# Performance work log

Measured on AMD Instinct MI355X. Metric: run time of the kernel, lower is better.

Reference implementation:

```python
import jax, jax.numpy as jnp
import numpy as np

INPUT_SIZE = 4096
HIDDEN = 1024
WINDOW = 2048
STRIDE = 1024
METRIC = 32
POOLING = "last"


def setup_inputs() -> dict:
    key = jax.random.key(0)
    ks = jax.random.split(key, 9)
    s = 1.0 / np.sqrt(HIDDEN)  # torch LSTMCell/Linear init bound
    u = lambda k, shape: jax.random.uniform(k, shape, jnp.float32, -s, s)
    return {
        "inp": jax.random.normal(ks[0], (WINDOW, INPUT_SIZE), jnp.float32),
        "h1": jax.random.normal(ks[1], (1, HIDDEN), jnp.float32),
        "c1": jax.random.normal(ks[2], (1, HIDDEN), jnp.float32),
        "W_ih": u(ks[3], (4 * HIDDEN, INPUT_SIZE)),
        "W_hh": u(ks[4], (4 * HIDDEN, HIDDEN)),
        "b_ih": u(ks[5], (4 * HIDDEN,)),
        "b_hh": u(ks[6], (4 * HIDDEN,)),
        "fc_w": u(ks[7], (METRIC, HIDDEN)),
        "fc_b": u(ks[8], (METRIC,)),
    }


def reference(inp, h1, c1, W_ih, W_hh, b_ih, b_hh, fc_w, fc_b):
    window = min(WINDOW, inp.shape[0])
    # Precompute the input-side gate projection as one GEMM: [T, 4H]
    xg = inp[:window] @ W_ih.T + b_ih

    def step(carry, xg_t):
        h, c = carry  # each [1, H]
        gates = xg_t + h @ W_hh.T + b_hh  # [1, 4H]
        i, f, g, o = jnp.split(gates, 4, axis=-1)
        c = jax.nn.sigmoid(f) * c + jax.nn.sigmoid(i) * jnp.tanh(g)
        h = jax.nn.sigmoid(o) * jnp.tanh(c)
        return (h, c), (h, c)

    (h_fin, c_fin), (hs, cs) = jax.lax.scan(step, (h1, c1), xg)

    if window >= STRIDE:
        h_last = jax.lax.stop_gradient(hs[STRIDE - 1])  # [1, H], detached
        c_last = jax.lax.stop_gradient(cs[STRIDE - 1])
    else:
        h_last, c_last = None, None

    if POOLING == "mean":
        # mean of fc(h_i) over last STRIDE steps of the window
        out = (hs[window - STRIDE:, 0, :] @ fc_w.T + fc_b).sum(axis=0, keepdims=True) / STRIDE
    else:  # 'last'
        out = h_fin @ fc_w.T + fc_b  # [1, METRIC]
    out = jnp.tanh(out)
    return out, h_last, c_last
```

## Files before the change

kernel.cpp:

```cpp
#include <hip/hip_runtime.h>
#include <stdint.h>

typedef unsigned short u16;
typedef unsigned long long u64;
typedef __attribute__((ext_vector_type(8))) short short8;
typedef __attribute__((ext_vector_type(4))) float floatx4;

#define K_IN    4096
#define HID     1024
#define G4H     4096
#define T_STEPS 2048
#define NWG     128
#define SPIN_MAX 60000

__device__ __forceinline__ u16 f2bf(float f) {
  union { float f; unsigned int i; } v; v.f = f;
  unsigned int lsb = (v.i >> 16) & 1u;
  v.i += 0x7fffu + lsb;
  return (u16)(v.i >> 16);
}
__device__ __forceinline__ float finz(float x) {
  unsigned b = __float_as_uint(x);
  return ((b & 0x7f800000u) == 0x7f800000u) ? 0.f : x;
}
__device__ __forceinline__ float sigm(float x) {
  x = fminf(30.f, fmaxf(-30.f, finz(x)));
  return 1.0f / (1.0f + __expf(-x));
}
__device__ __forceinline__ float tanh_s(float x) {
  x = fminf(15.f, fmaxf(-15.f, finz(x)));
  float e = __expf(2.0f * x);
  return (e - 1.0f) / (e + 1.0f);
}

__device__ __forceinline__ void publish_h(u64* hx, int slot, int idx, float h) {
  h = finz(h);
  u64 v = ((u64)(unsigned)(slot + 1) << 32) | (u64)__float_as_uint(h);
  __hip_atomic_store(&hx[(size_t)slot * HID + idx], v,
                     __ATOMIC_RELAXED, __HIP_MEMORY_SCOPE_AGENT);
}

#define HXLD(addr) __hip_atomic_load((addr), __ATOMIC_RELAXED, __HIP_MEMORY_SCOPE_AGENT)

__device__ __forceinline__ void poll2(const u64* hx, int slot, int j0,
                                      float* v, int* alive) {
  const u64* p = hx + (size_t)slot * HID + j0;
  const unsigned tag = (unsigned)(slot + 1);
  if (*alive) {
    u64 a0 = HXLD(&p[0]), b0 = HXLD(&p[1]);
    u64 a1 = HXLD(&p[0]), b1 = HXLD(&p[1]);
    int spins = 0;
    for (;;) {
      u64 a2 = HXLD(&p[0]), b2 = HXLD(&p[1]);
      if ((unsigned)(a0 >> 32) == tag && (unsigned)(b0 >> 32) == tag) {
        v[0] = finz(__uint_as_float((unsigned)a0));
        v[1] = finz(__uint_as_float((unsigned)b0));
        return;
      }
      a0 = a1; b0 = b1; a1 = a2; b1 = b2;
      if (++spins > SPIN_MAX) { *alive = 0; break; }
    }
  }
  v[0] = v[1] = 0.f;
}

__global__ __launch_bounds__(256) void cvt_bf16_k(const float* __restrict__ src,
                                                  u16* __restrict__ dst, int n4) {
  int i = blockIdx.x * 256 + threadIdx.x;
  if (i < n4) {
    float4 v = *(const float4*)(src + (size_t)i * 4);
    u16 o0 = f2bf(v.x), o1 = f2bf(v.y), o2 = f2bf(v.z), o3 = f2bf(v.w);
    ushort4 o = {o0, o1, o2, o3};
    *(ushort4*)(dst + (size_t)i * 4) = o;
  }
}

__global__ __launch_bounds__(256) void xg_gemm_k(const u16* __restrict__ A,
                                                 const u16* __restrict__ B,
                                                 const float* __restrict__ bias,
                                                 float* __restrict__ C)
{
  __shared__ __align__(16) u16 As[128 * 64];
  __shared__ __align__(16) u16 Bs[128 * 64];
  const int tid  = threadIdx.x;
  const int lane = tid & 63;
  const int quad = lane >> 4;
  const int l16  = lane & 15;
  const int wid  = tid >> 6;
  const int wm   = wid >> 1, wn = wid & 1;
  const int tileM = blockIdx.y * 128;
  const int tileN = blockIdx.x * 128;

  floatx4 acc[4][4];
  #pragma unroll
  for (int mi = 0; mi < 4; ++mi)
    #pragma unroll
    for (int ni = 0; ni < 4; ++ni)
      acc[mi][ni] = (floatx4){0.f, 0.f, 0.f, 0.f};

  for (int k0 = 0; k0 < K_IN; k0 += 64) {
    #pragma unroll
    for (int i = 0; i < 4; ++i) {
      int c = i * 256 + tid;
      int row = c >> 3, col = (c & 7) * 8;
      *(short8*)(As + c * 8) = *(const short8*)(A + (size_t)(tileM + row) * K_IN + k0 + col);
      *(short8*)(Bs + c * 8) = *(const short8*)(B + (size_t)(tileN + row) * K_IN + k0 + col);
    }
    __syncthreads();
    #pragma unroll
    for (int kk = 0; kk < 64; kk += 32) {
      short8 av[4], bv[4];
      #pragma unroll
      for (int mi = 0; mi < 4; ++mi)
        av[mi] = *(const short8*)(As + (wm * 64 + mi * 16 + l16) * 64 + kk + quad * 8);
      #pragma unroll
      for (int ni = 0; ni < 4; ++ni)
        bv[ni] = *(const short8*)(Bs + (wn * 64 + ni * 16 + l16) * 64 + kk + quad * 8);
      #pragma unroll
      for (int mi = 0; mi < 4; ++mi)
        #pragma unroll
        for (int ni = 0; ni < 4; ++ni)
          acc[mi][ni] = __builtin_amdgcn_mfma_f32_16x16x32_bf16(av[mi], bv[ni], acc[mi][ni], 0, 0, 0);
    }
    __syncthreads();
  }
  #pragma unroll
  for (int ni = 0; ni < 4; ++ni) {
    int n = tileN + wn * 64 + ni * 16 + l16;
    float bn = bias[n];
    #pragma unroll
    for (int mi = 0; mi < 4; ++mi) {
      int mbase = tileM + wm * 64 + mi * 16 + quad * 4;
      #pragma unroll
      for (int r = 0; r < 4; ++r)
        C[(size_t)(mbase + r) * G4H + n] = acc[mi][ni][r] + bn;
    }
  }
}

__global__ __launch_bounds__(512, 1) void lstm_scan_k(const float* __restrict__ Whh,
                                                      const float* __restrict__ bhh,
                                                      const float* __restrict__ h1,
                                                      const float* __restrict__ c1,
                                                      const float* __restrict__ fcw,
                                                      const float* __restrict__ fcb,
                                                      const float* __restrict__ xg,
                                                      u64* hx,
                                                      float* out)
{
  const int g    = blockIdx.x;
  const int tid  = threadIdx.x;
  const int lane = tid & 63;
  const int w    = tid >> 6;
  const int u    = g * 8 + w;

  __shared__ __align__(16) float h_local[HID];
  __shared__ float gsum2[32];
  __shared__ float xgb[2][32];
  __shared__ float bhhb[32];
  __shared__ float pp[32][16];

  floatx4 wreg[4][4];
  #pragma unroll
  for (int q = 0; q < 4; ++q) {
    const float* wr = Whh + (size_t)(q * HID + u) * HID;
    #pragma unroll
    for (int j = 0; j < 4; ++j)
      wreg[q][j] = *(const floatx4*)(wr + j * 256 + lane * 4);
  }
  if (tid < 32) bhhb[tid] = bhh[(tid >> 3) * HID + g * 8 + (tid & 7)];

  float c_state = 0.f;
  if (tid < 8) {
    c_state = c1[g * 8 + tid];
    publish_h(hx, 0, g * 8 + tid, h1[g * 8 + tid]);
  }

  int alive = 1;
  const int j0 = tid * 2;
  for (int t = 0; t < T_STEPS; ++t) {
    float xval = 0.f;
    if (tid < 32) xval = finz(xg[(size_t)t * G4H + (tid >> 3) * HID + g * 8 + (tid & 7)]);
    float v[2];
    poll2(hx, t, j0, v, &alive);
    h_local[j0 + 0] = v[0]; h_local[j0 + 1] = v[1];
    if (tid < 32) xgb[t & 1][tid] = xval;
    __syncthreads();

    float s0 = 0.f, s1 = 0.f, s2 = 0.f, s3 = 0.f;
    #pragma unroll
    for (int j = 0; j < 4; ++j) {
      floatx4 hv = *(const floatx4*)(h_local + j * 256 + lane * 4);
      #pragma unroll
      for (int k = 0; k < 4; ++k) {
        s0 = fmaf(wreg[0][j][k], hv[k], s0);
        s1 = fmaf(wreg[1][j][k], hv[k], s1);
        s2 = fmaf(wreg[2][j][k], hv[k], s2);
        s3 = fmaf(wreg[3][j][k], hv[k], s3);
      }
    }

#define DPP_LEVEL(mods) \
    asm("v_add_f32 %0, %0, %0 " mods : "+v"(s0)); \
    asm("v_add_f32 %0, %0, %0 " mods : "+v"(s1)); \
    asm("v_add_f32 %0, %0, %0 " mods : "+v"(s2)); \
    asm("v_add_f32 %0, %0, %0 " mods : "+v"(s3));
    DPP_LEVEL("row_shr:1 bound_ctrl:0")
    DPP_LEVEL("row_shr:2 bound_ctrl:0")
    DPP_LEVEL("row_shr:4 bank_mask:0xe")
    DPP_LEVEL("row_shr:8 bank_mask:0xc")
    DPP_LEVEL("row_bcast:15 row_mask:0xa")
    DPP_LEVEL("row_bcast:31 row_mask:0xc")
#undef DPP_LEVEL
    if (lane == 63) {
      gsum2[w * 4 + 0] = s0;
      gsum2[w * 4 + 1] = s1;
      gsum2[w * 4 + 2] = s2;
      gsum2[w * 4 + 3] = s3;
    }
    __syncthreads();

    if (tid < 8) {
      const int uu = tid;
      const float* xb = xgb[t & 1];
      float gi = gsum2[uu * 4 + 0] + xb[uu]      + bhhb[uu];
      float gf = gsum2[uu * 4 + 1] + xb[8 + uu]  + bhhb[8 + uu];
      float gg = gsum2[uu * 4 + 2] + xb[16 + uu] + bhhb[16 + uu];
      float go = gsum2[uu * 4 + 3] + xb[24 + uu] + bhhb[24 + uu];
      float iv = sigm(gi), fv = sigm(gf), gv = tanh_s(gg), ov = sigm(go);
      c_state = finz(fv * c_state + iv * gv);
      float hval = ov * tanh_s(c_state);
      publish_h(hx, t + 1, g * 8 + uu, hval);
      if (t == 1023) {
        out[32 + g * 8 + uu]       = finz(hval);
        out[32 + HID + g * 8 + uu] = finz(c_state);
      }
    }
  }

  if (g == 0) {
    float v[2];
    poll2(hx, T_STEPS, j0, v, &alive);
    h_local[j0 + 0] = v[0]; h_local[j0 + 1] = v[1];
    __syncthreads();
    const int m = tid >> 4, seg = tid & 15;
    float pacc = 0.f;
    for (int k = seg * 64; k < seg * 64 + 64; ++k)
      pacc = fmaf(fcw[m * HID + k], h_local[k], pacc);
    pp[m][seg] = finz(pacc);
    __syncthreads();
    if (tid < 32) {
      float sum = fcb[tid];
      #pragma unroll
      for (int i = 0; i < 16; ++i) sum += pp[tid][i];
      out[tid] = tanh_s(finz(sum));
    }
  }
}

extern "C" void kernel_launch(void* const* d_in, const int* in_sizes, int n_in,
                              void* d_out, int out_size, void* d_ws, size_t ws_size,
                              hipStream_t stream) {
  const float* inp = (const float*)d_in[0];
  const float* h1  = (const float*)d_in[1];
  const float* c1  = (const float*)d_in[2];
  const float* Wih = (const float*)d_in[3];
  const float* Whh = (const float*)d_in[4];
  const float* bih = (const float*)d_in[5];
  const float* bhh = (const float*)d_in[6];
  const float* fcw = (const float*)d_in[7];
  const float* fcb = (const float*)d_in[8];
  float* out = (float*)d_out;

  const size_t xg_bytes  = (size_t)T_STEPS * G4H * 4;
  const size_t hx_bytes  = (size_t)(T_STEPS + 1) * HID * 8;
  const size_t ab_bytes  = (size_t)T_STEPS * K_IN * 2;
  const size_t wb_bytes  = (size_t)G4H * K_IN * 2;
  if (ws_size < xg_bytes + hx_bytes + ab_bytes + wb_bytes) return;

  float* xg   = (float*)d_ws;
  u64*   hx   = (u64*)((char*)d_ws + xg_bytes);
  u16*   Abf  = (u16*)((char*)d_ws + xg_bytes + hx_bytes);
  u16*   Wbf  = (u16*)((char*)d_ws + xg_bytes + hx_bytes + ab_bytes);

  const int nA4 = T_STEPS * K_IN / 4;
  const int nW4 = G4H * K_IN / 4;
  cvt_bf16_k<<<dim3((nA4 + 255) / 256), 256, 0, stream>>>(inp, Abf, nA4);
  cvt_bf16_k<<<dim3((nW4 + 255) / 256), 256, 0, stream>>>(Wih, Wbf, nW4);
  xg_gemm_k<<<dim3(G4H / 128, T_STEPS / 128), 256, 0, stream>>>(Abf, Wbf, bih, xg);
  lstm_scan_k<<<dim3(NWG), 512, 0, stream>>>(Whh, bhh, h1, c1, fcw, fcb, xg, hx, out);
}
```

Baseline: 5.171 ms.

## Add per-workgroup ready flags and sleep-based polling to LSTM step sync

Each workgroup now publishes a compact per-step ready flag after writing its hidden values. At the start of each step, 128 threads spin on those flags with s_sleep backoff before the whole block reads the tagged h entries. The hidden-state poll loop drops its pipelined triple-load pattern in favour of a plain load plus s_sleep. The goal is to cut memory-system contention from 512 threads spinning on 8KB of h values, at the cost of an extra barrier and a second dependent round-trip per step. The flag array reuses the bf16 input buffer after the GEMM has consumed it.

```diff
diff --git a/kernel.cpp b/kernel.cpp
--- a/kernel.cpp
+++ b/kernel.cpp
@@ -2,6 +2,7 @@
 #include <stdint.h>
 
 typedef unsigned short u16;
+typedef unsigned int u32;
 typedef unsigned long long u64;
 typedef __attribute__((ext_vector_type(8))) short short8;
 typedef __attribute__((ext_vector_type(4))) float floatx4;
@@ -40,28 +41,38 @@
                      __ATOMIC_RELAXED, __HIP_MEMORY_SCOPE_AGENT);
 }
 
-#define HXLD(addr) __hip_atomic_load((addr), __ATOMIC_RELAXED, __HIP_MEMORY_SCOPE_AGENT)
-
 __device__ __forceinline__ void poll2(const u64* hx, int slot, int j0,
                                       float* v, int* alive) {
   const u64* p = hx + (size_t)slot * HID + j0;
   const unsigned tag = (unsigned)(slot + 1);
   if (*alive) {
-    u64 a0 = HXLD(&p[0]), b0 = HXLD(&p[1]);
-    u64 a1 = HXLD(&p[0]), b1 = HXLD(&p[1]);
     int spins = 0;
     for (;;) {
-      u64 a2 = HXLD(&p[0]), b2 = HXLD(&p[1]);
-      if ((unsigned)(a0 >> 32) == tag && (unsigned)(b0 >> 32) == tag) {
-        v[0] = finz(__uint_as_float((unsigned)a0));
-        v[1] = finz(__uint_as_float((unsigned)b0));
+      u64 a = __hip_atomic_load(&p[0], __ATOMIC_RELAXED, __HIP_MEMORY_SCOPE_AGENT);
+      u64 b = __hip_atomic_load(&p[1], __ATOMIC_RELAXED, __HIP_MEMORY_SCOPE_AGENT);
+      if ((unsigned)(a >> 32) == tag && (unsigned)(b >> 32) == tag) {
+        v[0] = finz(__uint_as_float((unsigned)a));
+        v[1] = finz(__uint_as_float((unsigned)b));
         return;
       }
-      a0 = a1; b0 = b1; a1 = a2; b1 = b2;
       if (++spins > SPIN_MAX) { *alive = 0; break; }
+      __builtin_amdgcn_s_sleep(1);
     }
   }
   v[0] = v[1] = 0.f;
+}
+
+__device__ __forceinline__ void flag_wait(const u32* flags, int slot, int i,
+                                          int* alive) {
+  const u32* p = flags + (size_t)slot * NWG + i;
+  const unsigned tag = (unsigned)(slot + 1);
+  if (*alive) {
+    int spins = 0;
+    while (__hip_atomic_load(p, __ATOMIC_RELAXED, __HIP_MEMORY_SCOPE_AGENT) != tag) {
+      if (++spins > SPIN_MAX) { *alive = 0; break; }
+      __builtin_amdgcn_s_sleep(1);
+    }
+  }
 }
 
 __global__ __launch_bounds__(256) void cvt_bf16_k(const float* __restrict__ src,
@@ -146,6 +157,7 @@
                                                       const float* __restrict__ fcb,
                                                       const float* __restrict__ xg,
                                                       u64* hx,
+                                                      u32* flags,
                                                       float* out)
 {
   const int g    = blockIdx.x;
@@ -175,12 +187,18 @@
     c_state = c1[g * 8 + tid];
     publish_h(hx, 0, g * 8 + tid, h1[g * 8 + tid]);
   }
+  if (tid == 0)
+    __hip_atomic_store(&flags[g], 1u, __ATOMIC_RELAXED, __HIP_MEMORY_SCOPE_AGENT);
 
   int alive = 1;
   const int j0 = tid * 2;
   for (int t = 0; t < T_STEPS; ++t) {
     float xval = 0.f;
     if (tid < 32) xval = finz(xg[(size_t)t * G4H + (tid >> 3) * HID + g * 8 + (tid & 7)]);
+
+    if (tid < NWG) flag_wait(flags, t, tid, &alive);
+    __syncthreads();
+
     float v[2];
     poll2(hx, t, j0, v, &alive);
     h_local[j0 + 0] = v[0]; h_local[j0 + 1] = v[1];
@@ -236,6 +254,9 @@
         out[32 + HID + g * 8 + uu] = finz(c_state);
       }
     }
+    if (tid == 0)
+      __hip_atomic_store(&flags[(size_t)(t + 1) * NWG + g], (unsigned)(t + 2),
+                         __ATOMIC_RELAXED, __HIP_MEMORY_SCOPE_AGENT);
   }
 
   if (g == 0) {
@@ -282,11 +303,12 @@
   u64*   hx   = (u64*)((char*)d_ws + xg_bytes);
   u16*   Abf  = (u16*)((char*)d_ws + xg_bytes + hx_bytes);
   u16*   Wbf  = (u16*)((char*)d_ws + xg_bytes + hx_bytes + ab_bytes);
+  u32*   flags = (u32*)Abf;
 
   const int nA4 = T_STEPS * K_IN / 4;
   const int nW4 = G4H * K_IN / 4;
   cvt_bf16_k<<<dim3((nA4 + 255) / 256), 256, 0, stream>>>(inp, Abf, nA4);
   cvt_bf16_k<<<dim3((nW4 + 255) / 256), 256, 0, stream>>>(Wih, Wbf, nW4);
   xg_gemm_k<<<dim3(G4H / 128, T_STEPS / 128), 256, 0, stream>>>(Abf, Wbf, bih, xg);
-  lstm_scan_k<<<dim3(NWG), 512, 0, stream>>>(Whh, bhh, h1, c1, fcw, fcb, xg, hx, out);
-}
+  lstm_scan_k<<<dim3(NWG), 512, 0, stream>>>(Whh, bhh, h1, c1, fcw, fcb, xg, hx, flags, out);
+}
```

After: 7.826 ms. 1.51x slower.
